# Performance work log

Hardware: AMD Instinct MI355X
Metric: run time of the kernel (lower is better)

The kernel has to match this reference:

```python
import jax, jax.numpy as jnp
import numpy as np

KS = 3          # ksize
PAD = 1         # (ksize-1)//2 * dilation, dilation=1

def setup_inputs() -> dict:
    key = jax.random.key(0)
    k1, k2, k3, k4 = jax.random.split(key, 4)
    B, NI, C, H, W = 4, 64, 64, 256, 256
    features = jax.random.normal(k1, (B, NI, H, W), jnp.float32)
    inpt = jax.random.normal(k2, (B, C, H, W), jnp.float32)
    # get_filter: Conv2d(ni, ksize**2, 3, padding=1 reflect, stride=1)
    w = jax.random.normal(k3, (KS * KS, NI, 3, 3), jnp.float32) * 0.05
    b = jax.random.normal(k4, (KS * KS,), jnp.float32) * 0.01
    return {"features": features, "inpt": inpt, "w": w, "b": b}

def reference(features, inpt, w, b):
    # 1) predict per-pixel filters: 3x3 conv with reflect padding
    fpad = jnp.pad(features, ((0, 0), (0, 0), (1, 1), (1, 1)), mode="reflect")
    ff = jax.lax.conv_general_dilated(
        fpad, w, window_strides=(1, 1), padding="VALID",
        dimension_numbers=("NCHW", "OIHW", "NCHW"),
    ) + b[None, :, None, None]                       # [B, 9, H, W]
    ff = jax.nn.softmax(ff, axis=1)                  # softmax over the 9 taps

    # 2) apply per-pixel filter to inpt (shared across channels)
    B, C, H, W = inpt.shape
    ipad = jnp.pad(inpt, ((0, 0), (0, 0), (PAD, PAD), (PAD, PAD)), mode="reflect")
    # unfold: taps in row-major (ki, kj) order, matching torch nn.Unfold
    patches = jnp.stack(
        [ipad[:, :, i:i + H, j:j + W] for i in range(KS) for j in range(KS)],
        axis=2,
    )                                                # [B, C, 9, H, W]
    # out[b,c,h,w] = sum_k patches[b,c,k,h,w] * ff[b,k,h,w]
    return jnp.einsum("bckhw,bkhw->bchw", patches, ff)
```

## Files before the change

### kernel.cpp

```cpp
#include <hip/hip_runtime.h>
#include <math.h>

#define BB 4
#define NI 64
#define CC 64
#define HH 256
#define WW 256
#define HW (HH * WW)

#define SRW 68
#define BUFW 272
#define NBUF 2

__device__ __forceinline__ int refl(int i, int n) {
    i = (i < 0) ? -i : i;
    return (i >= n) ? (2 * n - 2 - i) : i;
}

__global__ __launch_bounds__(512) void pff_wave(
    const float* __restrict__ features,
    const float* __restrict__ inpt,
    const float* __restrict__ wgt,
    const float* __restrict__ bias,
    float* __restrict__ out)
{
    __shared__ float stage[8][NBUF * BUFW];
    __shared__ float part[2][9][256];

    const int tid  = threadIdx.x;
    const int wv   = __builtin_amdgcn_readfirstlane(tid >> 6);
    const int half = wv >> 2;
    const int tr   = wv & 3;
    const int l    = tid & 63;
    const int p    = tid & 255;
    const int W0 = blockIdx.x * 64;
    const int H0 = blockIdx.y * 8;
    const int b  = blockIdx.z;

    int goff[5], loff[5];
    #pragma unroll
    for (int t = 0; t < 5; ++t) {
        const int e = (t < 4) ? (l + 64 * t) : (256 + (l & 7));
        const int row = e / 66, col = e - row * 66;
        loff[t] = row * SRW + col;
        goff[t] = refl(H0 + 2 * tr - 1 + row, HH) * WW + refl(W0 - 1 + col, WW);
    }
    const bool do5 = (l < 8);

    float accA[9], accB[9];
    #pragma unroll
    for (int k = 0; k < 9; ++k) { accA[k] = 0.f; accB[k] = 0.f; }

    float* sb = &stage[wv][0];

    const float* fb = features + (size_t)b * NI * HW + (size_t)half * 32 * HW;
    float r0 = fb[goff[0]], r1 = fb[goff[1]], r2 = fb[goff[2]], r3 = fb[goff[3]];
    float r4 = do5 ? fb[goff[4]] : 0.f;

    for (int ni = 0; ni < 32; ++ni) {
        float* bw = sb + (ni & 1) * BUFW;
        bw[loff[0]] = r0; bw[loff[1]] = r1; bw[loff[2]] = r2; bw[loff[3]] = r3;
        if (do5) bw[loff[4]] = r4;
        if (ni < 31) {
            const float* fn = fb + (size_t)(ni + 1) * HW;
            r0 = fn[goff[0]]; r1 = fn[goff[1]]; r2 = fn[goff[2]]; r3 = fn[goff[3]];
            if (do5) r4 = fn[goff[4]];
        }

        float f[12];
        #pragma unroll
        for (int rr = 0; rr < 4; ++rr) {
            const float* br = bw + rr * SRW + l;
            f[rr * 3 + 0] = br[0];
            f[rr * 3 + 1] = br[1];
            f[rr * 3 + 2] = br[2];
        }

        const float* wn = wgt + (half * 32 + ni) * 9;
        #pragma unroll
        for (int k = 0; k < 9; ++k) {
            const float* wk = wn + k * (NI * 9);
            const float w0 = wk[0], w1 = wk[1], w2 = wk[2];
            const float w3 = wk[3], w4 = wk[4], w5 = wk[5];
            const float w6 = wk[6], w7 = wk[7], w8 = wk[8];
            accA[k] = fmaf(f[0],  w0, accA[k]);
            accB[k] = fmaf(f[3],  w0, accB[k]);
            accA[k] = fmaf(f[1],  w1, accA[k]);
            accB[k] = fmaf(f[4],  w1, accB[k]);
            accA[k] = fmaf(f[2],  w2, accA[k]);
            accB[k] = fmaf(f[5],  w2, accB[k]);
            accA[k] = fmaf(f[3],  w3, accA[k]);
            accB[k] = fmaf(f[6],  w3, accB[k]);
            accA[k] = fmaf(f[4],  w4, accA[k]);
            accB[k] = fmaf(f[7],  w4, accB[k]);
            accA[k] = fmaf(f[5],  w5, accA[k]);
            accB[k] = fmaf(f[8],  w5, accB[k]);
            accA[k] = fmaf(f[6],  w6, accA[k]);
            accB[k] = fmaf(f[9],  w6, accB[k]);
            accA[k] = fmaf(f[7],  w7, accA[k]);
            accB[k] = fmaf(f[10], w7, accB[k]);
            accA[k] = fmaf(f[8],  w8, accA[k]);
            accB[k] = fmaf(f[11], w8, accB[k]);
        }
    }

    const float* ib = inpt + (size_t)b * CC * HW + (size_t)half * 32 * HW;
    r0 = ib[goff[0]]; r1 = ib[goff[1]]; r2 = ib[goff[2]]; r3 = ib[goff[3]];
    if (do5) r4 = ib[goff[4]];

    #pragma unroll
    for (int k = 0; k < 9; ++k) part[half][k][p] = accA[k];
    __syncthreads();
    #pragma unroll
    for (int k = 0; k < 9; ++k) accA[k] = part[0][k][p] + part[1][k][p] + bias[k];
    __syncthreads();
    #pragma unroll
    for (int k = 0; k < 9; ++k) part[half][k][p] = accB[k];
    __syncthreads();
    #pragma unroll
    for (int k = 0; k < 9; ++k) accB[k] = part[0][k][p] + part[1][k][p] + bias[k];

    {
        float m = accA[0];
        #pragma unroll
        for (int k = 1; k < 9; ++k) m = fmaxf(m, accA[k]);
        float s = 0.f;
        #pragma unroll
        for (int k = 0; k < 9; ++k) { accA[k] = __expf(accA[k] - m); s += accA[k]; }
        const float inv = 1.f / s;
        #pragma unroll
        for (int k = 0; k < 9; ++k) accA[k] *= inv;
    }
    {
        float m = accB[0];
        #pragma unroll
        for (int k = 1; k < 9; ++k) m = fmaxf(m, accB[k]);
        float s = 0.f;
        #pragma unroll
        for (int k = 0; k < 9; ++k) { accB[k] = __expf(accB[k] - m); s += accB[k]; }
        const float inv = 1.f / s;
        #pragma unroll
        for (int k = 0; k < 9; ++k) accB[k] *= inv;
    }

    float* ob = out + (size_t)b * CC * HW + (size_t)half * 32 * HW;
    const int oA = (H0 + 2 * tr) * WW + W0 + l;
    const int oB = oA + WW;

    for (int ch = 0; ch < 32; ++ch) {
        float* bw = sb + (ch & 1) * BUFW;
        bw[loff[0]] = r0; bw[loff[1]] = r1; bw[loff[2]] = r2; bw[loff[3]] = r3;
        if (do5) bw[loff[4]] = r4;
        if (ch < 31) {
            const float* in2 = ib + (size_t)(ch + 1) * HW;
            r0 = in2[goff[0]]; r1 = in2[goff[1]]; r2 = in2[goff[2]]; r3 = in2[goff[3]];
            if (do5) r4 = in2[goff[4]];
        }

        float f[12];
        #pragma unroll
        for (int rr = 0; rr < 4; ++rr) {
            const float* br = bw + rr * SRW + l;
            f[rr * 3 + 0] = br[0];
            f[rr * 3 + 1] = br[1];
            f[rr * 3 + 2] = br[2];
        }

        float vA = accA[0] * f[0];
        float vB = accB[0] * f[3];
        vA = fmaf(accA[1], f[1],  vA);  vB = fmaf(accB[1], f[4],  vB);
        vA = fmaf(accA[2], f[2],  vA);  vB = fmaf(accB[2], f[5],  vB);
        vA = fmaf(accA[3], f[3],  vA);  vB = fmaf(accB[3], f[6],  vB);
        vA = fmaf(accA[4], f[4],  vA);  vB = fmaf(accB[4], f[7],  vB);
        vA = fmaf(accA[5], f[5],  vA);  vB = fmaf(accB[5], f[8],  vB);
        vA = fmaf(accA[6], f[6],  vA);  vB = fmaf(accB[6], f[9],  vB);
        vA = fmaf(accA[7], f[7],  vA);  vB = fmaf(accB[7], f[10], vB);
        vA = fmaf(accA[8], f[8],  vA);  vB = fmaf(accB[8], f[11], vB);
        ob[(size_t)ch * HW + oA] = vA;
        ob[(size_t)ch * HW + oB] = vB;
    }
}

extern "C" void kernel_launch(void* const* d_in, const int* in_sizes, int n_in,
                              void* d_out, int out_size, void* d_ws, size_t ws_size,
                              hipStream_t stream) {
    const float* features = (const float*)d_in[0];
    const float* inpt     = (const float*)d_in[1];
    const float* wgt      = (const float*)d_in[2];
    const float* bias     = (const float*)d_in[3];
    float* out            = (float*)d_out;

    dim3 grid(WW / 64, HH / 8, BB);
    dim3 block(512);
    pff_wave<<<grid, block, 0, stream>>>(features, inpt, wgt, bias, out);
}
```

Before: 70.30 us.

## Stage conv weights in LDS and prefetch two channels ahead

Copies all filter-predictor weights into shared memory, padded to 12-float rows, at kernel start. The inner conv loop then reads them with float4 LDS loads, with the next tap's weights fetched ahead, instead of scalar global loads. Both channel loops are unrolled by two so global loads for channel n+2 and n+3 are in flight while the current channels are computed. This adds about 27KB of LDS and extra registers, which may reduce occupancy.

```diff
diff --git a/kernel.cpp b/kernel.cpp
--- a/kernel.cpp
+++ b/kernel.cpp
@@ -2,7 +2,7 @@
 #include <math.h>
 
 #define BB 4
-#define NI 64
+#define NIC 64
 #define CC 64
 #define HH 256
 #define WW 256
@@ -10,21 +10,59 @@
 
 #define SRW 68
 #define BUFW 272
-#define NBUF 2
+#define WROW 12
 
 __device__ __forceinline__ int refl(int i, int n) {
     i = (i < 0) ? -i : i;
     return (i >= n) ? (2 * n - 2 - i) : i;
 }
 
-__global__ __launch_bounds__(512) void pff_wave(
+__device__ __forceinline__ void kfma(const float* __restrict__ wl,
+                                     const float f[12],
+                                     float accA[9], float accB[9]) {
+    float4 q0 = *reinterpret_cast<const float4*>(wl);
+    float4 q1 = *reinterpret_cast<const float4*>(wl + 4);
+    float w8 = wl[8];
+    #pragma unroll
+    for (int k = 0; k < 9; ++k) {
+        float4 n0, n1; float n8 = 0.f;
+        if (k < 8) {
+            const float* wn = wl + (k + 1) * WROW;
+            n0 = *reinterpret_cast<const float4*>(wn);
+            n1 = *reinterpret_cast<const float4*>(wn + 4);
+            n8 = wn[8];
+        }
+        accA[k] = fmaf(f[0],  q0.x, accA[k]);
+        accB[k] = fmaf(f[3],  q0.x, accB[k]);
+        accA[k] = fmaf(f[1],  q0.y, accA[k]);
+        accB[k] = fmaf(f[4],  q0.y, accB[k]);
+        accA[k] = fmaf(f[2],  q0.z, accA[k]);
+        accB[k] = fmaf(f[5],  q0.z, accB[k]);
+        accA[k] = fmaf(f[3],  q0.w, accA[k]);
+        accB[k] = fmaf(f[6],  q0.w, accB[k]);
+        accA[k] = fmaf(f[4],  q1.x, accA[k]);
+        accB[k] = fmaf(f[7],  q1.x, accB[k]);
+        accA[k] = fmaf(f[5],  q1.y, accA[k]);
+        accB[k] = fmaf(f[8],  q1.y, accB[k]);
+        accA[k] = fmaf(f[6],  q1.z, accA[k]);
+        accB[k] = fmaf(f[9],  q1.z, accB[k]);
+        accA[k] = fmaf(f[7],  q1.w, accA[k]);
+        accB[k] = fmaf(f[10], q1.w, accB[k]);
+        accA[k] = fmaf(f[8],  w8, accA[k]);
+        accB[k] = fmaf(f[11], w8, accB[k]);
+        if (k < 8) { q0 = n0; q1 = n1; w8 = n8; }
+    }
+}
+
+__global__ __launch_bounds__(512) void pff_wavew(
     const float* __restrict__ features,
     const float* __restrict__ inpt,
     const float* __restrict__ wgt,
     const float* __restrict__ bias,
     float* __restrict__ out)
 {
-    __shared__ float stage[8][NBUF * BUFW];
+    __shared__ float stage[8][2 * BUFW];
+    __shared__ float wlds[NIC * 9 * WROW];
     __shared__ float part[2][9][256];
 
     const int tid  = threadIdx.x;
@@ -37,6 +75,14 @@
     const int H0 = blockIdx.y * 8;
     const int b  = blockIdx.z;
 
+    for (int d = tid; d < NIC * 9 * WROW; d += 512) {
+        const int ni = d / (9 * WROW);
+        const int r  = d - ni * 9 * WROW;
+        const int k  = r / WROW;
+        const int s  = r - k * WROW;
+        wlds[d] = (s < 9) ? wgt[k * 576 + ni * 9 + s] : 0.f;
+    }
+
     int goff[5], loff[5];
     #pragma unroll
     for (int t = 0; t < 5; ++t) {
@@ -52,61 +98,62 @@
     for (int k = 0; k < 9; ++k) { accA[k] = 0.f; accB[k] = 0.f; }
 
     float* sb = &stage[wv][0];
-
-    const float* fb = features + (size_t)b * NI * HW + (size_t)half * 32 * HW;
-    float r0 = fb[goff[0]], r1 = fb[goff[1]], r2 = fb[goff[2]], r3 = fb[goff[3]];
-    float r4 = do5 ? fb[goff[4]] : 0.f;
-
-    for (int ni = 0; ni < 32; ++ni) {
-        float* bw = sb + (ni & 1) * BUFW;
-        bw[loff[0]] = r0; bw[loff[1]] = r1; bw[loff[2]] = r2; bw[loff[3]] = r3;
-        if (do5) bw[loff[4]] = r4;
-        if (ni < 31) {
-            const float* fn = fb + (size_t)(ni + 1) * HW;
-            r0 = fn[goff[0]]; r1 = fn[goff[1]]; r2 = fn[goff[2]]; r3 = fn[goff[3]];
-            if (do5) r4 = fn[goff[4]];
-        }
-
-        float f[12];
-        #pragma unroll
-        for (int rr = 0; rr < 4; ++rr) {
-            const float* br = bw + rr * SRW + l;
-            f[rr * 3 + 0] = br[0];
-            f[rr * 3 + 1] = br[1];
-            f[rr * 3 + 2] = br[2];
-        }
-
-        const float* wn = wgt + (half * 32 + ni) * 9;
-        #pragma unroll
-        for (int k = 0; k < 9; ++k) {
-            const float* wk = wn + k * (NI * 9);
-            const float w0 = wk[0], w1 = wk[1], w2 = wk[2];
-            const float w3 = wk[3], w4 = wk[4], w5 = wk[5];
-            const float w6 = wk[6], w7 = wk[7], w8 = wk[8];
-            accA[k] = fmaf(f[0],  w0, accA[k]);
-            accB[k] = fmaf(f[3],  w0, accB[k]);
-            accA[k] = fmaf(f[1],  w1, accA[k]);
-            accB[k] = fmaf(f[4],  w1, accB[k]);
-            accA[k] = fmaf(f[2],  w2, accA[k]);
-            accB[k] = fmaf(f[5],  w2, accB[k]);
-            accA[k] = fmaf(f[3],  w3, accA[k]);
-            accB[k] = fmaf(f[6],  w3, accB[k]);
-            accA[k] = fmaf(f[4],  w4, accA[k]);
-            accB[k] = fmaf(f[7],  w4, accB[k]);
-            accA[k] = fmaf(f[5],  w5, accA[k]);
-            accB[k] = fmaf(f[8],  w5, accB[k]);
-            accA[k] = fmaf(f[6],  w6, accA[k]);
-            accB[k] = fmaf(f[9],  w6, accB[k]);
-            accA[k] = fmaf(f[7],  w7, accA[k]);
-            accB[k] = fmaf(f[10], w7, accB[k]);
-            accA[k] = fmaf(f[8],  w8, accA[k]);
-            accB[k] = fmaf(f[11], w8, accB[k]);
+    __syncthreads();
+
+    const float* fb = features + (size_t)b * NIC * HW + (size_t)half * 32 * HW;
+    float a0 = fb[goff[0]], a1 = fb[goff[1]], a2 = fb[goff[2]], a3 = fb[goff[3]];
+    float a4 = do5 ? fb[goff[4]] : 0.f;
+    const float* fb1 = fb + HW;
+    float b0 = fb1[goff[0]], b1 = fb1[goff[1]], b2 = fb1[goff[2]], b3 = fb1[goff[3]];
+    float b4 = do5 ? fb1[goff[4]] : 0.f;
+
+    for (int ni = 0; ni < 32; ni += 2) {
+        {
+            float* bw = sb;
+            bw[loff[0]] = a0; bw[loff[1]] = a1; bw[loff[2]] = a2; bw[loff[3]] = a3;
+            if (do5) bw[loff[4]] = a4;
+            if (ni + 2 < 32) {
+                const float* fn = fb + (size_t)(ni + 2) * HW;
+                a0 = fn[goff[0]]; a1 = fn[goff[1]]; a2 = fn[goff[2]]; a3 = fn[goff[3]];
+                if (do5) a4 = fn[goff[4]];
+            }
+            float f[12];
+            #pragma unroll
+            for (int rr = 0; rr < 4; ++rr) {
+                const float* br = bw + rr * SRW + l;
+                f[rr * 3 + 0] = br[0];
+                f[rr * 3 + 1] = br[1];
+                f[rr * 3 + 2] = br[2];
+            }
+            kfma(&wlds[(half * 32 + ni) * 9 * WROW], f, accA, accB);
+        }
+        {
+            float* bw = sb + BUFW;
+            bw[loff[0]] = b0; bw[loff[1]] = b1; bw[loff[2]] = b2; bw[loff[3]] = b3;
+            if (do5) bw[loff[4]] = b4;
+            if (ni + 3 < 32) {
+                const float* fn = fb + (size_t)(ni + 3) * HW;
+                b0 = fn[goff[0]]; b1 = fn[goff[1]]; b2 = fn[goff[2]]; b3 = fn[goff[3]];
+                if (do5) b4 = fn[goff[4]];
+            }
+            float f[12];
+            #pragma unroll
+            for (int rr = 0; rr < 4; ++rr) {
+                const float* br = bw + rr * SRW + l;
+                f[rr * 3 + 0] = br[0];
+                f[rr * 3 + 1] = br[1];
+                f[rr * 3 + 2] = br[2];
+            }
+            kfma(&wlds[(half * 32 + ni + 1) * 9 * WROW], f, accA, accB);
         }
     }
 
     const float* ib = inpt + (size_t)b * CC * HW + (size_t)half * 32 * HW;
-    r0 = ib[goff[0]]; r1 = ib[goff[1]]; r2 = ib[goff[2]]; r3 = ib[goff[3]];
-    if (do5) r4 = ib[goff[4]];
+    a0 = ib[goff[0]]; a1 = ib[goff[1]]; a2 = ib[goff[2]]; a3 = ib[goff[3]];
+    if (do5) a4 = ib[goff[4]];
+    const float* ib1 = ib + HW;
+    b0 = ib1[goff[0]]; b1 = ib1[goff[1]]; b2 = ib1[goff[2]]; b3 = ib1[goff[3]];
+    if (do5) b4 = ib1[goff[4]];
 
     #pragma unroll
     for (int k = 0; k < 9; ++k) part[half][k][p] = accA[k];
@@ -147,37 +194,67 @@
     const int oA = (H0 + 2 * tr) * WW + W0 + l;
     const int oB = oA + WW;
 
-    for (int ch = 0; ch < 32; ++ch) {
-        float* bw = sb + (ch & 1) * BUFW;
-        bw[loff[0]] = r0; bw[loff[1]] = r1; bw[loff[2]] = r2; bw[loff[3]] = r3;
-        if (do5) bw[loff[4]] = r4;
-        if (ch < 31) {
-            const float* in2 = ib + (size_t)(ch + 1) * HW;
-            r0 = in2[goff[0]]; r1 = in2[goff[1]]; r2 = in2[goff[2]]; r3 = in2[goff[3]];
-            if (do5) r4 = in2[goff[4]];
-        }
-
-        float f[12];
-        #pragma unroll
-        for (int rr = 0; rr < 4; ++rr) {
-            const float* br = bw + rr * SRW + l;
-            f[rr * 3 + 0] = br[0];
-            f[rr * 3 + 1] = br[1];
-            f[rr * 3 + 2] = br[2];
-        }
-
-        float vA = accA[0] * f[0];
-        float vB = accB[0] * f[3];
-        vA = fmaf(accA[1], f[1],  vA);  vB = fmaf(accB[1], f[4],  vB);
-        vA = fmaf(accA[2], f[2],  vA);  vB = fmaf(accB[2], f[5],  vB);
-        vA = fmaf(accA[3], f[3],  vA);  vB = fmaf(accB[3], f[6],  vB);
-        vA = fmaf(accA[4], f[4],  vA);  vB = fmaf(accB[4], f[7],  vB);
-        vA = fmaf(accA[5], f[5],  vA);  vB = fmaf(accB[5], f[8],  vB);
-        vA = fmaf(accA[6], f[6],  vA);  vB = fmaf(accB[6], f[9],  vB);
-        vA = fmaf(accA[7], f[7],  vA);  vB = fmaf(accB[7], f[10], vB);
-        vA = fmaf(accA[8], f[8],  vA);  vB = fmaf(accB[8], f[11], vB);
-        ob[(size_t)ch * HW + oA] = vA;
-        ob[(size_t)ch * HW + oB] = vB;
+    for (int ch = 0; ch < 32; ch += 2) {
+        {
+            float* bw = sb;
+            bw[loff[0]] = a0; bw[loff[1]] = a1; bw[loff[2]] = a2; bw[loff[3]] = a3;
+            if (do5) bw[loff[4]] = a4;
+            if (ch + 2 < 32) {
+                const float* in2 = ib + (size_t)(ch + 2) * HW;
+                a0 = in2[goff[0]]; a1 = in2[goff[1]]; a2 = in2[goff[2]]; a3 = in2[goff[3]];
+                if (do5) a4 = in2[goff[4]];
+            }
+            float f[12];
+            #pragma unroll
+            for (int rr = 0; rr < 4; ++rr) {
+                const float* br = bw + rr * SRW + l;
+                f[rr * 3 + 0] = br[0];
+                f[rr * 3 + 1] = br[1];
+                f[rr * 3 + 2] = br[2];
+            }
+            float vA = accA[0] * f[0];
+            float vB = accB[0] * f[3];
+            vA = fmaf(accA[1], f[1],  vA);  vB = fmaf(accB[1], f[4],  vB);
+            vA = fmaf(accA[2], f[2],  vA);  vB = fmaf(accB[2], f[5],  vB);
+            vA = fmaf(accA[3], f[3],  vA);  vB = fmaf(accB[3], f[6],  vB);
+            vA = fmaf(accA[4], f[4],  vA);  vB = fmaf(accB[4], f[7],  vB);
+            vA = fmaf(accA[5], f[5],  vA);  vB = fmaf(accB[5], f[8],  vB);
+            vA = fmaf(accA[6], f[6],  vA);  vB = fmaf(accB[6], f[9],  vB);
+            vA = fmaf(accA[7], f[7],  vA);  vB = fmaf(accB[7], f[10], vB);
+            vA = fmaf(accA[8], f[8],  vA);  vB = fmaf(accB[8], f[11], vB);
+            ob[(size_t)ch * HW + oA] = vA;
+            ob[(size_t)ch * HW + oB] = vB;
+        }
+        {
+            float* bw = sb + BUFW;
+            bw[loff[0]] = b0; bw[loff[1]] = b1; bw[loff[2]] = b2; bw[loff[3]] = b3;
+            if (do5) bw[loff[4]] = b4;
+            if (ch + 3 < 32) {
+                const float* in2 = ib + (size_t)(ch + 3) * HW;
+                b0 = in2[goff[0]]; b1 = in2[goff[1]]; b2 = in2[goff[2]]; b3 = in2[goff[3]];
+                if (do5) b4 = in2[goff[4]];
+            }
+            float f[12];
+            #pragma unroll
+            for (int rr = 0; rr < 4; ++rr) {
+                const float* br = bw + rr * SRW + l;
+                f[rr * 3 + 0] = br[0];
+                f[rr * 3 + 1] = br[1];
+                f[rr * 3 + 2] = br[2];
+            }
+            float vA = accA[0] * f[0];
+            float vB = accB[0] * f[3];
+            vA = fmaf(accA[1], f[1],  vA);  vB = fmaf(accB[1], f[4],  vB);
+            vA = fmaf(accA[2], f[2],  vA);  vB = fmaf(accB[2], f[5],  vB);
+            vA = fmaf(accA[3], f[3],  vA);  vB = fmaf(accB[3], f[6],  vB);
+            vA = fmaf(accA[4], f[4],  vA);  vB = fmaf(accB[4], f[7],  vB);
+            vA = fmaf(accA[5], f[5],  vA);  vB = fmaf(accB[5], f[8],  vB);
+            vA = fmaf(accA[6], f[6],  vA);  vB = fmaf(accB[6], f[9],  vB);
+            vA = fmaf(accA[7], f[7],  vA);  vB = fmaf(accB[7], f[10], vB);
+            vA = fmaf(accA[8], f[8],  vA);  vB = fmaf(accB[8], f[11], vB);
+            ob[(size_t)(ch + 1) * HW + oA] = vA;
+            ob[(size_t)(ch + 1) * HW + oB] = vB;
+        }
     }
 }
 
@@ -192,5 +269,5 @@
 
     dim3 grid(WW / 64, HH / 8, BB);
     dim3 block(512);
-    pff_wave<<<grid, block, 0, stream>>>(features, inpt, wgt, bias, out);
-}
+    pff_wavew<<<grid, block, 0, stream>>>(features, inpt, wgt, bias, out);
+}
```

New measurement: 98.57 us. 1.4x slower.
